# Performance work log

Measured on AMD Instinct MI355X. Metric: run time of the kernel, lower is better.

Reference implementation:

```python
import jax, jax.numpy as jnp
import numpy as np

IN_FEATURES = 4096
OUT_FEATURES = 11008
BATCH = 16


def setup_inputs() -> dict:
    key = jax.random.key(0)
    k_x, k_w, k_s, k_b = jax.random.split(key, 4)
    x = jax.random.normal(k_x, (BATCH, IN_FEATURES), dtype=jnp.float32)
    # symmetric int8 weights stored as int32 for jax portability (values in [-127, 127])
    weight_int8 = jax.random.randint(k_w, (OUT_FEATURES, IN_FEATURES), -127, 128, dtype=jnp.int32)
    # per-output-channel scales, small positive values typical of int8 quantization
    weight_scale = jax.random.uniform(k_s, (OUT_FEATURES,), dtype=jnp.float32, minval=0.005, maxval=0.02)
    bias = jax.random.normal(k_b, (OUT_FEATURES,), dtype=jnp.float32)
    return {"x": x, "weight_int8": weight_int8, "weight_scale": weight_scale, "bias": bias}


def reference(x, weight_int8, weight_scale, bias):
    # Dequantize: w_dq[o, i] = int8[o, i] * scale[o]  -> fp32 [OUT, IN]
    w_dq = weight_int8.astype(x.dtype) * weight_scale[:, None]
    # F.linear: y = x @ w_dq.T + bias  -> [BATCH, OUT]
    return jnp.einsum("bi,oi->bo", x, w_dq) + bias
```

## Files before the change

### kernel.cpp

```cpp
#include <hip/hip_runtime.h>

#define IN_F   4096
#define OUT_F  11008
#define BATCH  16
#define BLOCK  256
#define SPLITK 8
#define KCHUNK (IN_F / SPLITK)
#define NSTEP  (KCHUNK / 32)

typedef short s16x8 __attribute__((ext_vector_type(8)));
typedef float f32x4 __attribute__((ext_vector_type(4)));
typedef int   i32x4 __attribute__((ext_vector_type(4)));
typedef unsigned short u16;

__device__ __forceinline__ u16 f32_to_bf16_rne(float f) {
    unsigned u = __float_as_uint(f);
    unsigned r = u + 0x7FFFu + ((u >> 16) & 1u);
    return (u16)(r >> 16);
}
__device__ __forceinline__ float bf16_bits_to_f32(u16 h) {
    return __uint_as_float((unsigned)h << 16);
}

__global__ __launch_bounds__(BLOCK) void prep_kernel(
    const float* __restrict__ x, const float* __restrict__ bias,
    float* __restrict__ out, u16* __restrict__ xhi, u16* __restrict__ xlo)
{
    const int bid = blockIdx.x;
    const int tid = threadIdx.x;
    if (bid < (BATCH * IN_F) / BLOCK) {
        int i = bid * BLOCK + tid;
        float v  = x[i];
        u16 h    = f32_to_bf16_rne(v);
        float hf = bf16_bits_to_f32(h);
        u16 l    = f32_to_bf16_rne(v - hf);
        xhi[i] = h;
        xlo[i] = l;
    } else {
        int i = (bid - (BATCH * IN_F) / BLOCK) * BLOCK + tid;
        out[i] = bias[i % OUT_F];
    }
}

__global__ __launch_bounds__(BLOCK) void qlin_kernel(
    const int*   __restrict__ w,
    const float* __restrict__ scale,
    const u16*   __restrict__ xhi,
    const u16*   __restrict__ xlo,
    float* __restrict__ out)
{
    const int tid  = threadIdx.x;
    const int lane = tid & 63;
    const int wv   = tid >> 6;
    const int n    = lane & 15;
    const int quad = lane >> 4;
    const int o0   = blockIdx.x * 64 + wv * 16;
    const int kb   = blockIdx.y * KCHUNK;

    const int* __restrict__ wrow = w   + (size_t)(o0 + n) * IN_F + kb + quad * 8;
    const u16* __restrict__ xh   = xhi + n * IN_F + kb + quad * 8;
    const u16* __restrict__ xl   = xlo + n * IN_F + kb + quad * 8;

    i32x4 wa[2], wb[2];
    s16x8 ah[2], al[2];
    wa[0] = __builtin_nontemporal_load((const i32x4*)wrow);
    wb[0] = __builtin_nontemporal_load((const i32x4*)(wrow + 4));
    ah[0] = *(const s16x8*)xh;
    al[0] = *(const s16x8*)xl;

    f32x4 acc = {0.f, 0.f, 0.f, 0.f};

    #pragma unroll
    for (int s = 0; s < NSTEP; ++s) {
        const int cur = s & 1, nxt = cur ^ 1;
        if (s + 1 < NSTEP) {
            wa[nxt] = __builtin_nontemporal_load((const i32x4*)(wrow + (s + 1) * 32));
            wb[nxt] = __builtin_nontemporal_load((const i32x4*)(wrow + (s + 1) * 32 + 4));
            ah[nxt] = *(const s16x8*)(xh + (s + 1) * 32);
            al[nxt] = *(const s16x8*)(xl + (s + 1) * 32);
        }

        s16x8 bfrag;
        #pragma unroll
        for (int e = 0; e < 4; ++e) {
            bfrag[e]     = (short)(u16)(__float_as_uint((float)wa[cur][e]) >> 16);
            bfrag[4 + e] = (short)(u16)(__float_as_uint((float)wb[cur][e]) >> 16);
        }

        acc = __builtin_amdgcn_mfma_f32_16x16x32_bf16(ah[cur], bfrag, acc, 0, 0, 0);
        acc = __builtin_amdgcn_mfma_f32_16x16x32_bf16(al[cur], bfrag, acc, 0, 0, 0);
    }

    const int   o  = o0 + n;
    const float sc = scale[o];
    #pragma unroll
    for (int r = 0; r < 4; ++r) {
        const int b = quad * 4 + r;
        atomicAdd(&out[(size_t)b * OUT_F + o], acc[r] * sc);
    }
}

extern "C" void kernel_launch(void* const* d_in, const int* in_sizes, int n_in,
                              void* d_out, int out_size, void* d_ws, size_t ws_size,
                              hipStream_t stream) {
    const float* x     = (const float*)d_in[0];
    const int*   w     = (const int*)d_in[1];
    const float* scale = (const float*)d_in[2];
    const float* bias  = (const float*)d_in[3];
    float* out = (float*)d_out;

    u16* xhi = (u16*)d_ws;
    u16* xlo = (u16*)((char*)d_ws + BATCH * IN_F * sizeof(u16));

    prep_kernel<<<(BATCH * IN_F) / BLOCK + (BATCH * OUT_F) / BLOCK, BLOCK, 0, stream>>>(
        x, bias, out, xhi, xlo);

    dim3 grid(OUT_F / 64, SPLITK);
    qlin_kernel<<<grid, dim3(BLOCK), 0, stream>>>(w, scale, xhi, xlo, out);
}
```

Measured before the change: 266.3 us.

## Pack int32 weights to int8 in prep kernel and load all K-chunk weights upfront

The prep kernel now converts the int32 weight matrix into a packed int8 copy in the workspace, and the GEMM kernel reads those packed bytes. The GEMM kernel also issues all of its chunk's weight loads up front, then runs four MFMAs per iteration over 64 K elements. The goal is to shrink the weight bytes the GEMM streams and to raise memory-level parallelism. The cost is that the full int32 matrix is still read and a packed copy is written on every call, which adds traffic.

Measured after the change: 275.8 us. 3.6% more time.

```diff
diff --git a/kernel.cpp b/kernel.cpp
--- a/kernel.cpp
+++ b/kernel.cpp
@@ -6,7 +6,7 @@
 #define BLOCK  256
 #define SPLITK 8
 #define KCHUNK (IN_F / SPLITK)
-#define NSTEP  (KCHUNK / 32)
+#define NITER  (KCHUNK / 64)
 
 typedef short s16x8 __attribute__((ext_vector_type(8)));
 typedef float f32x4 __attribute__((ext_vector_type(4)));
@@ -21,32 +21,48 @@
 __device__ __forceinline__ float bf16_bits_to_f32(u16 h) {
     return __uint_as_float((unsigned)h << 16);
 }
+__device__ __forceinline__ short bf16_trunc(float f) {
+    return (short)(u16)(__float_as_uint(f) >> 16);
+}
 
 __global__ __launch_bounds__(BLOCK) void prep_kernel(
-    const float* __restrict__ x, const float* __restrict__ bias,
-    float* __restrict__ out, u16* __restrict__ xhi, u16* __restrict__ xlo)
+    const float* __restrict__ x, const int* __restrict__ w,
+    const float* __restrict__ bias, float* __restrict__ out,
+    unsigned char* __restrict__ wp, u16* __restrict__ xhi, u16* __restrict__ xlo)
 {
     const int bid = blockIdx.x;
     const int tid = threadIdx.x;
-    if (bid < (BATCH * IN_F) / BLOCK) {
-        int i = bid * BLOCK + tid;
+    if (bid < OUT_F) {
+        const i32x4* __restrict__ src = (const i32x4*)(w + (size_t)bid * IN_F);
+        unsigned* __restrict__ dst = (unsigned*)(wp + (size_t)bid * IN_F);
+        #pragma unroll
+        for (int j = 0; j < 4; ++j) {
+            int g = tid + j * BLOCK;
+            i32x4 v = __builtin_nontemporal_load(src + g);
+            unsigned p = (unsigned)(v[0] & 0xFF)
+                       | ((unsigned)(v[1] & 0xFF) << 8)
+                       | ((unsigned)(v[2] & 0xFF) << 16)
+                       | ((unsigned)(v[3] & 0xFF) << 24);
+            dst[g] = p;
+        }
+    } else if (bid < OUT_F + (BATCH * IN_F) / BLOCK) {
+        int i = (bid - OUT_F) * BLOCK + tid;
         float v  = x[i];
         u16 h    = f32_to_bf16_rne(v);
-        float hf = bf16_bits_to_f32(h);
-        u16 l    = f32_to_bf16_rne(v - hf);
+        u16 l    = f32_to_bf16_rne(v - bf16_bits_to_f32(h));
         xhi[i] = h;
         xlo[i] = l;
     } else {
-        int i = (bid - (BATCH * IN_F) / BLOCK) * BLOCK + tid;
+        int i = (bid - OUT_F - (BATCH * IN_F) / BLOCK) * BLOCK + tid;
         out[i] = bias[i % OUT_F];
     }
 }
 
 __global__ __launch_bounds__(BLOCK) void qlin_kernel(
-    const int*   __restrict__ w,
+    const unsigned char* __restrict__ wp,
     const float* __restrict__ scale,
-    const u16*   __restrict__ xhi,
-    const u16*   __restrict__ xlo,
+    const u16* __restrict__ xhi,
+    const u16* __restrict__ xlo,
     float* __restrict__ out)
 {
     const int tid  = threadIdx.x;
@@ -57,38 +73,42 @@
     const int o0   = blockIdx.x * 64 + wv * 16;
     const int kb   = blockIdx.y * KCHUNK;
 
-    const int* __restrict__ wrow = w   + (size_t)(o0 + n) * IN_F + kb + quad * 8;
-    const u16* __restrict__ xh   = xhi + n * IN_F + kb + quad * 8;
-    const u16* __restrict__ xl   = xlo + n * IN_F + kb + quad * 8;
+    const i32x4* __restrict__ wrow =
+        (const i32x4*)(wp + (size_t)(o0 + n) * IN_F + kb + quad * 16);
 
-    i32x4 wa[2], wb[2];
-    s16x8 ah[2], al[2];
-    wa[0] = __builtin_nontemporal_load((const i32x4*)wrow);
-    wb[0] = __builtin_nontemporal_load((const i32x4*)(wrow + 4));
-    ah[0] = *(const s16x8*)xh;
-    al[0] = *(const s16x8*)xl;
+    i32x4 wq[NITER];
+    #pragma unroll
+    for (int t = 0; t < NITER; ++t)
+        wq[t] = __builtin_nontemporal_load(wrow + t * 4);
+
+    const u16* __restrict__ xh = xhi + n * IN_F + kb + quad * 16;
+    const u16* __restrict__ xl = xlo + n * IN_F + kb + quad * 16;
 
     f32x4 acc = {0.f, 0.f, 0.f, 0.f};
 
     #pragma unroll
-    for (int s = 0; s < NSTEP; ++s) {
-        const int cur = s & 1, nxt = cur ^ 1;
-        if (s + 1 < NSTEP) {
-            wa[nxt] = __builtin_nontemporal_load((const i32x4*)(wrow + (s + 1) * 32));
-            wb[nxt] = __builtin_nontemporal_load((const i32x4*)(wrow + (s + 1) * 32 + 4));
-            ah[nxt] = *(const s16x8*)(xh + (s + 1) * 32);
-            al[nxt] = *(const s16x8*)(xl + (s + 1) * 32);
+    for (int t = 0; t < NITER; ++t) {
+        s16x8 ahlo = *(const s16x8*)(xh + t * 64);
+        s16x8 ahhi = *(const s16x8*)(xh + t * 64 + 8);
+        s16x8 allo = *(const s16x8*)(xl + t * 64);
+        s16x8 alhi = *(const s16x8*)(xl + t * 64 + 8);
+
+        s16x8 blo, bhi;
+        #pragma unroll
+        for (int e = 0; e < 2; ++e) {
+            int v1 = wq[t][e];
+            int v2 = wq[t][2 + e];
+            #pragma unroll
+            for (int b = 0; b < 4; ++b) {
+                blo[e * 4 + b] = bf16_trunc((float)((v1 << (24 - 8 * b)) >> 24));
+                bhi[e * 4 + b] = bf16_trunc((float)((v2 << (24 - 8 * b)) >> 24));
+            }
         }
 
-        s16x8 bfrag;
-        #pragma unroll
-        for (int e = 0; e < 4; ++e) {
-            bfrag[e]     = (short)(u16)(__float_as_uint((float)wa[cur][e]) >> 16);
-            bfrag[4 + e] = (short)(u16)(__float_as_uint((float)wb[cur][e]) >> 16);
-        }
-
-        acc = __builtin_amdgcn_mfma_f32_16x16x32_bf16(ah[cur], bfrag, acc, 0, 0, 0);
-        acc = __builtin_amdgcn_mfma_f32_16x16x32_bf16(al[cur], bfrag, acc, 0, 0, 0);
+        acc = __builtin_amdgcn_mfma_f32_16x16x32_bf16(ahlo, blo, acc, 0, 0, 0);
+        acc = __builtin_amdgcn_mfma_f32_16x16x32_bf16(allo, blo, acc, 0, 0, 0);
+        acc = __builtin_amdgcn_mfma_f32_16x16x32_bf16(ahhi, bhi, acc, 0, 0, 0);
+        acc = __builtin_amdgcn_mfma_f32_16x16x32_bf16(alhi, bhi, acc, 0, 0, 0);
     }
 
     const int   o  = o0 + n;
@@ -109,12 +129,13 @@
     const float* bias  = (const float*)d_in[3];
     float* out = (float*)d_out;
 
-    u16* xhi = (u16*)d_ws;
-    u16* xlo = (u16*)((char*)d_ws + BATCH * IN_F * sizeof(u16));
+    unsigned char* wp = (unsigned char*)d_ws;
+    u16* xhi = (u16*)(wp + (size_t)OUT_F * IN_F);
+    u16* xlo = xhi + BATCH * IN_F;
 
-    prep_kernel<<<(BATCH * IN_F) / BLOCK + (BATCH * OUT_F) / BLOCK, BLOCK, 0, stream>>>(
-        x, bias, out, xhi, xlo);
+    const int PREP_BLOCKS = OUT_F + (BATCH * IN_F) / BLOCK + (BATCH * OUT_F) / BLOCK;
+    prep_kernel<<<PREP_BLOCKS, BLOCK, 0, stream>>>(x, w, bias, out, wp, xhi, xlo);
 
     dim3 grid(OUT_F / 64, SPLITK);
-    qlin_kernel<<<grid, dim3(BLOCK), 0, stream>>>(w, scale, xhi, xlo, out);
+    qlin_kernel<<<grid, dim3(BLOCK), 0, stream>>>(wp, scale, xhi, xlo, out);
 }
```

## Issue all weight loads upfront and double split-K to deepen memory parallelism

Applied to the files above, without the earlier changes.

Raises split-K from 8 to 16, which halves each block's K chunk and doubles the grid. Each thread now issues all of its weight vector loads for that chunk before any compute, replacing the one-step-ahead double buffer. The goal is more bytes in flight per wave and more waves overall, so the memory-bound int32 weight stream can saturate HBM. The cost is higher register pressure from 16 i32x4 registers and twice as many atomicAdds to the output, and the loads lose their nontemporal hint.

Result: faster. 260.7 us (-2.1%).

```diff
diff --git a/kernel.cpp b/kernel.cpp
--- a/kernel.cpp
+++ b/kernel.cpp
@@ -4,7 +4,7 @@
 #define OUT_F  11008
 #define BATCH  16
 #define BLOCK  256
-#define SPLITK 8
+#define SPLITK 16
 #define KCHUNK (IN_F / SPLITK)
 #define NSTEP  (KCHUNK / 32)
 
@@ -21,6 +21,9 @@
 __device__ __forceinline__ float bf16_bits_to_f32(u16 h) {
     return __uint_as_float((unsigned)h << 16);
 }
+__device__ __forceinline__ short bf16_trunc(float f) {
+    return (short)(u16)(__float_as_uint(f) >> 16);
+}
 
 __global__ __launch_bounds__(BLOCK) void prep_kernel(
     const float* __restrict__ x, const float* __restrict__ bias,
@@ -32,8 +35,7 @@
         int i = bid * BLOCK + tid;
         float v  = x[i];
         u16 h    = f32_to_bf16_rne(v);
-        float hf = bf16_bits_to_f32(h);
-        u16 l    = f32_to_bf16_rne(v - hf);
+        u16 l    = f32_to_bf16_rne(v - bf16_bits_to_f32(h));
         xhi[i] = h;
         xlo[i] = l;
     } else {
@@ -57,38 +59,45 @@
     const int o0   = blockIdx.x * 64 + wv * 16;
     const int kb   = blockIdx.y * KCHUNK;
 
-    const int* __restrict__ wrow = w   + (size_t)(o0 + n) * IN_F + kb + quad * 8;
-    const u16* __restrict__ xh   = xhi + n * IN_F + kb + quad * 8;
-    const u16* __restrict__ xl   = xlo + n * IN_F + kb + quad * 8;
+    const i32x4* __restrict__ wbase =
+        (const i32x4*)(w + (size_t)(o0 + n) * IN_F + kb);
+    const int qb = quad * 2;
 
-    i32x4 wa[2], wb[2];
-    s16x8 ah[2], al[2];
-    wa[0] = __builtin_nontemporal_load((const i32x4*)wrow);
-    wb[0] = __builtin_nontemporal_load((const i32x4*)(wrow + 4));
-    ah[0] = *(const s16x8*)xh;
-    al[0] = *(const s16x8*)xl;
+    i32x4 wq[2 * NSTEP];
+    #pragma unroll
+    for (int s = 0; s < NSTEP; ++s) {
+        wq[2 * s]     = wbase[s * 8 + qb];
+        wq[2 * s + 1] = wbase[s * 8 + qb + 1];
+    }
+
+    const u16* __restrict__ xh = xhi + n * IN_F + kb + quad * 8;
+    const u16* __restrict__ xl = xlo + n * IN_F + kb + quad * 8;
 
     f32x4 acc = {0.f, 0.f, 0.f, 0.f};
 
+    s16x8 ah = *(const s16x8*)xh;
+    s16x8 al = *(const s16x8*)xl;
+
     #pragma unroll
     for (int s = 0; s < NSTEP; ++s) {
-        const int cur = s & 1, nxt = cur ^ 1;
+        s16x8 ah2, al2;
         if (s + 1 < NSTEP) {
-            wa[nxt] = __builtin_nontemporal_load((const i32x4*)(wrow + (s + 1) * 32));
-            wb[nxt] = __builtin_nontemporal_load((const i32x4*)(wrow + (s + 1) * 32 + 4));
-            ah[nxt] = *(const s16x8*)(xh + (s + 1) * 32);
-            al[nxt] = *(const s16x8*)(xl + (s + 1) * 32);
+            ah2 = *(const s16x8*)(xh + (s + 1) * 32);
+            al2 = *(const s16x8*)(xl + (s + 1) * 32);
         }
 
         s16x8 bfrag;
         #pragma unroll
         for (int e = 0; e < 4; ++e) {
-            bfrag[e]     = (short)(u16)(__float_as_uint((float)wa[cur][e]) >> 16);
-            bfrag[4 + e] = (short)(u16)(__float_as_uint((float)wb[cur][e]) >> 16);
+            bfrag[e]     = bf16_trunc((float)wq[2 * s][e]);
+            bfrag[4 + e] = bf16_trunc((float)wq[2 * s + 1][e]);
         }
 
-        acc = __builtin_amdgcn_mfma_f32_16x16x32_bf16(ah[cur], bfrag, acc, 0, 0, 0);
-        acc = __builtin_amdgcn_mfma_f32_16x16x32_bf16(al[cur], bfrag, acc, 0, 0, 0);
+        acc = __builtin_amdgcn_mfma_f32_16x16x32_bf16(ah, bfrag, acc, 0, 0, 0);
+        acc = __builtin_amdgcn_mfma_f32_16x16x32_bf16(al, bfrag, acc, 0, 0, 0);
+
+        ah = ah2;
+        al = al2;
     }
 
     const int   o  = o0 + n;
@@ -110,10 +119,10 @@
     float* out = (float*)d_out;
 
     u16* xhi = (u16*)d_ws;
-    u16* xlo = (u16*)((char*)d_ws + BATCH * IN_F * sizeof(u16));
+    u16* xlo = xhi + BATCH * IN_F;
 
-    prep_kernel<<<(BATCH * IN_F) / BLOCK + (BATCH * OUT_F) / BLOCK, BLOCK, 0, stream>>>(
-        x, bias, out, xhi, xlo);
+    const int PREP_BLOCKS = (BATCH * IN_F) / BLOCK + (BATCH * OUT_F) / BLOCK;
+    prep_kernel<<<PREP_BLOCKS, BLOCK, 0, stream>>>(x, bias, out, xhi, xlo);
 
     dim3 grid(OUT_F / 64, SPLITK);
     qlin_kernel<<<grid, dim3(BLOCK), 0, stream>>>(w, scale, xhi, xlo, out);
```
